# Kernel optimization log

Hardware: AMD Instinct MI355X
Metric: run time of the kernel (lower is better)

The kernel has to match this reference:

```python
import jax, jax.numpy as jnp
import numpy as np

CHANNELS_CHOICE = np.array([8, 16, 24, 32, 40, 48, 56, 64])
MAX_C = 64
B, H, W_SP = 128, 32, 32
N_EDGES = 6
# edge list per intermediate node: (edge_weight_index, source_node_index)
EDGES = [[(0, 0)], [(1, 0), (2, 1)], [(3, 0), (4, 1), (5, 2)]]


def setup_inputs() -> dict:
    key = jax.random.key(0)
    k1, k2, k3, k4 = jax.random.split(key, 4)
    inputs = jax.random.normal(k1, (B, MAX_C, H, W_SP), dtype=jnp.float32)
    alphas1 = jax.random.uniform(k2, (8,), dtype=jnp.float32)  # input-width arch weights
    alphas2 = jax.random.uniform(k3, (8,), dtype=jnp.float32)  # output-width arch weights
    # shared master 3x3 conv weight per edge (OIHW)
    W = jax.random.normal(k4, (N_EDGES, MAX_C, MAX_C, 3, 3), dtype=jnp.float32) * 0.05
    return {"inputs": inputs, "alphas1": alphas1, "alphas2": alphas2, "W": W}


def _channel_scale(alphas1, alphas2, dtype):
    # mask[c, i] = 1 if channel c is inside width choice CHANNELS_CHOICE[i]
    mask = (jnp.arange(MAX_C)[:, None] < jnp.asarray(CHANNELS_CHOICE)[None, :]).astype(dtype)  # [64, 8]
    a_in = mask @ alphas1   # [64] cumulative input-channel weight
    a_out = mask @ alphas2  # [64] cumulative output-channel weight
    return a_out[:, None] * a_in[None, :]  # [64, 64]


def _edge(x, w, scale):
    # weighted-combi of all (c1, c2) channel-sliced sub-convs == one conv with scaled weight
    w_eff = w * scale[:, :, None, None]
    return jax.lax.conv_general_dilated(
        jax.nn.relu(x), w_eff, window_strides=(1, 1), padding="SAME",
        dimension_numbers=("NCHW", "OIHW", "NCHW"))


def reference(inputs, alphas1, alphas2, W):
    scale = _channel_scale(alphas1, alphas2, inputs.dtype)
    nodes = [inputs]
    for node_edges in EDGES:
        feat = 0.0
        for l, src in node_edges:
            feat = feat + _edge(nodes[src], W[l], scale)
        nodes.append(feat)
    return nodes[-1]
```

## Files before the change

kernel.cpp:

```cpp
#include <hip/hip_runtime.h>
#include <hip/hip_bf16.h>


typedef __bf16 bf16x8 __attribute__((ext_vector_type(8)));
typedef float floatx4 __attribute__((ext_vector_type(4)));
typedef unsigned int uint32;

#define PADW 34
#define PIMG (PADW * PADW)
#define ROWB (PADW * 64 * 2)
#define A_LDS (18 * ROWB)
#define A_CHUNKS (A_LDS / 16)
#define A_TAIL (A_CHUNKS - 9 * 512)
#define TAPB (64 * 64 * 2)
#define B_LDS (9 * TAPB)
#define SMEM_BYTES (A_LDS + B_LDS)

__device__ __forceinline__ void gld16(const char* g, char* l) {
    __builtin_amdgcn_global_load_lds(
        (const __attribute__((address_space(1))) uint32*)g,
        (__attribute__((address_space(3))) uint32*)l, 16, 0, 0);
}

__global__ __launch_bounds__(256) void pre_kernel(
    const float* __restrict__ in, const float* __restrict__ a1,
    const float* __restrict__ a2, const float* __restrict__ W,
    __hip_bfloat16* __restrict__ wt, __hip_bfloat16* __restrict__ r0,
    __hip_bfloat16* __restrict__ r1, __hip_bfloat16* __restrict__ r2) {
    __shared__ float tile[32][65];
    int blk = blockIdx.x;
    int tid = threadIdx.x;

    if (blk < 864) {
        int idx = blk * 256 + tid;
        int i = idx & 63;
        int o = (idx >> 6) & 63;
        int rest = idx >> 12;
        int t = rest % 9;
        int l = rest / 9;
        int ji = i >> 3, jo = o >> 3;
        float ain = 0.f, aout = 0.f;
#pragma unroll
        for (int j = 0; j < 8; ++j) {
            ain  += (j >= ji) ? a1[j] : 0.f;
            aout += (j >= jo) ? a2[j] : 0.f;
        }
        float v = W[(size_t)((l * 64 + o) * 64 + i) * 9 + t] * ain * aout;
        int os = ((o & 3) << 4) + (o >> 2);
        size_t e = (size_t)(l * 9 + t) * 4096 + os * 64 +
                   ((((i >> 3) ^ (os & 7)) << 3) + (i & 7));
        wt[e] = __float2bfloat16(v);
    } else if (blk < 992) {
        int b = blk - 864;
        __hip_bfloat16* bufs[3] = {r0, r1, r2};
#pragma unroll
        for (int f = 0; f < 3; ++f) {
            uint32* buf = (uint32*)(bufs[f] + (size_t)b * PIMG * 64);
            for (int idx = tid; idx < 132 * 32; idx += 256) {
                int slot = idx >> 5, u = idx & 31;
                int yy, xx;
                if (slot < 34)      { yy = 0;  xx = slot; }
                else if (slot < 68) { yy = 33; xx = slot - 34; }
                else { int s2 = slot - 68; yy = 1 + (s2 >> 1); xx = (s2 & 1) * 33; }
                buf[(size_t)(yy * PADW + xx) * 32 + u] = 0u;
            }
        }
    } else {
        int rb = blk - 992;
        int b = rb >> 5, y = rb & 31;
        int x = tid & 31, c0 = tid >> 5;
        const float* ip = in + ((size_t)b * 64 * 32 + y) * 32 + x;
#pragma unroll
        for (int cc = 0; cc < 8; ++cc) {
            int c = cc * 8 + c0;
            tile[x][c] = fmaxf(ip[(size_t)c * 1024], 0.f);
        }
        __syncthreads();
        int j = tid & 7, xq = tid >> 3;
        int p = (b * PADW + y + 1) * PADW + 1 + xq;
        alignas(16) __hip_bfloat16 hv[8];
#pragma unroll
        for (int k = 0; k < 8; ++k)
            hv[k] = __float2bfloat16(tile[xq][j * 8 + k]);
        *(uint4*)((char*)r0 + (size_t)p * 128 + ((j ^ (p & 7)) << 4)) =
            *(const uint4*)hv;
    }
}

template <int NSRC, bool FINAL>
__global__ __launch_bounds__(512, 1) void conv_stage(
    const __hip_bfloat16* __restrict__ s0,
    const __hip_bfloat16* __restrict__ s1,
    const __hip_bfloat16* __restrict__ s2,
    const __hip_bfloat16* __restrict__ wt,
    void* __restrict__ dstv, int l0) {
    extern __shared__ char smem[];
    char* smemB = smem + A_LDS;
    int tid = threadIdx.x;
    int wv = tid >> 6, lane = tid & 63;
    int quad = lane >> 4, l15 = lane & 15;
    int blk = blockIdx.x;
    int b = blk >> 1, y0 = (blk & 1) << 4;

    const char* srcs[3] = {(const char*)s0, (const char*)s1, (const char*)s2};
    const char* gW = (const char*)wt + (size_t)l0 * 9 * (size_t)TAPB;
    const size_t aOff = (size_t)(b * PADW + y0) * PADW * 128;

    auto stage_A = [&](int s) {
        const char* gA = srcs[s] + aOff;
#pragma unroll
        for (int it = 0; it < 10; ++it) {
            int c = it * 512 + tid;
            if (it < 9 || tid < A_TAIL)
                gld16(gA + (size_t)c * 16, smem + (it * 512 + wv * 64) * 16);
        }
    };
    auto stage_B = [&](int s) {
        const char* gB = gW + (size_t)s * 9 * TAPB;
#pragma unroll
        for (int it = 0; it < 9; ++it) {
            int c = it * 512 + tid;
            gld16(gB + (size_t)c * 16, smemB + (it * 512 + wv * 64) * 16);
        }
    };

    auto ldA = [&](int tl, int q, bf16x8 (&dst)[4]) {
        const int ky = tl / 3, kx = tl % 3;
#pragma unroll
        for (int m = 0; m < 4; ++m) {
            int arow = 2 * wv + (m >> 1) + ky;
            int apx  = ((m & 1) << 4) + l15 + kx;
            int R = b * PADW + y0 + arow;
            int slot = ((q << 2) + quad) ^ ((2 * R + apx) & 7);
            dst[m] = *(const bf16x8*)(smem + arow * ROWB + apx * 128 +
                                      slot * 16);
        }
    };
    auto ldB = [&](int tl, int q, bf16x8 (&dst)[4]) {
#pragma unroll
        for (int n = 0; n < 4; ++n) {
            int o = (n << 4) + l15;
            int slot = ((q << 2) + quad) ^ (l15 & 7);
            dst[n] = *(const bf16x8*)(smemB + tl * TAPB + o * 128 +
                                      slot * 16);
        }
    };

    floatx4 acc[4][4];
#pragma unroll
    for (int m = 0; m < 4; ++m)
#pragma unroll
        for (int n = 0; n < 4; ++n) acc[m][n] = (floatx4){0.f, 0.f, 0.f, 0.f};

    stage_A(0);
    stage_B(0);
    __syncthreads();

#pragma unroll 1
    for (int s = 0; s < NSRC; ++s) {
        bf16x8 fA[2][4], fB[2][4];
        ldA(0, 0, fA[0]);
        ldB(0, 0, fB[0]);
#pragma unroll
        for (int st = 0; st < 18; ++st) {
            const int pb = st & 1;
            if (st < 17) {
                const int nt = (st + 1) >> 1, nq = (st + 1) & 1;
                ldA(nt, nq, fA[pb ^ 1]);
                ldB(nt, nq, fB[pb ^ 1]);
            }
            __builtin_amdgcn_s_setprio(1);
#pragma unroll
            for (int m = 0; m < 4; ++m)
#pragma unroll
                for (int n = 0; n < 4; ++n)
                    acc[m][n] = __builtin_amdgcn_mfma_f32_16x16x32_bf16(
                        fA[pb][m], fB[pb][n], acc[m][n], 0, 0, 0);
            __builtin_amdgcn_s_setprio(0);
        }
        if (s + 1 < NSRC) {
            __syncthreads();
            stage_A(s + 1);
            stage_B(s + 1);
            __syncthreads();
        }
    }

    if (FINAL) {
        float* out = (float*)dstv;
#pragma unroll
        for (int m = 0; m < 4; ++m) {
            int row = y0 + 2 * wv + (m >> 1);
#pragma unroll
            for (int n = 0; n < 4; ++n) {
                int o = (l15 << 2) + n;
                *(floatx4*)(out + (((size_t)b * 64 + o) * 32 + row) * 32 +
                            ((m & 1) << 4) + (quad << 2)) = acc[m][n];
            }
        }
    } else {
        __hip_bfloat16* out = (__hip_bfloat16*)dstv;
#pragma unroll
        for (int m = 0; m < 4; ++m) {
            int row = y0 + 2 * wv + (m >> 1);
#pragma unroll
            for (int r = 0; r < 4; ++r) {
                int x = ((m & 1) << 4) + (quad << 2) + r;
                int p = (b * PADW + row + 1) * PADW + x + 1;
                alignas(8) __hip_bfloat16 hv[4];
#pragma unroll
                for (int n = 0; n < 4; ++n)
                    hv[n] = __float2bfloat16(fmaxf(acc[m][n][r], 0.f));
                char* d8 = (char*)out + (size_t)p * 128 +
                           ((((l15 >> 1) ^ (p & 7)) << 4) + ((l15 & 1) << 3));
                *(uint2*)d8 = *(const uint2*)hv;
            }
        }
    }
}

extern "C" void kernel_launch(void* const* d_in, const int* in_sizes, int n_in,
                              void* d_out, int out_size, void* d_ws,
                              size_t ws_size, hipStream_t stream) {
    const float* inputs  = (const float*)d_in[0];
    const float* alphas1 = (const float*)d_in[1];
    const float* alphas2 = (const float*)d_in[2];
    const float* W       = (const float*)d_in[3];
    char* ws = (char*)d_ws;

    __hip_bfloat16* wt = (__hip_bfloat16*)(ws);
    __hip_bfloat16* r0 = (__hip_bfloat16*)(ws + ((size_t)1 << 20));
    __hip_bfloat16* r1 = (__hip_bfloat16*)(ws + ((size_t)20 << 20));
    __hip_bfloat16* r2 = (__hip_bfloat16*)(ws + ((size_t)40 << 20));
    float* out = (float*)d_out;

    (void)hipFuncSetAttribute((const void*)conv_stage<1, false>,
                              hipFuncAttributeMaxDynamicSharedMemorySize,
                              SMEM_BYTES);
    (void)hipFuncSetAttribute((const void*)conv_stage<2, false>,
                              hipFuncAttributeMaxDynamicSharedMemorySize,
                              SMEM_BYTES);
    (void)hipFuncSetAttribute((const void*)conv_stage<3, true>,
                              hipFuncAttributeMaxDynamicSharedMemorySize,
                              SMEM_BYTES);

    pre_kernel<<<864 + 128 + 4096, 256, 0, stream>>>(inputs, alphas1, alphas2,
                                                     W, wt, r0, r1, r2);
    conv_stage<1, false><<<256, 512, SMEM_BYTES, stream>>>(r0, r1, r2, wt,
                                                           (void*)r1, 0);
    conv_stage<2, false><<<256, 512, SMEM_BYTES, stream>>>(r0, r1, r2, wt,
                                                           (void*)r2, 1);
    conv_stage<3, true ><<<256, 512, SMEM_BYTES, stream>>>(r0, r1, r2, wt,
                                                           (void*)out, 3);
}
```

Baseline: 148.9 us.

## Fuse input ReLU/bf16 padding conversion into first conv stage

The first conv stage now reads the fp32 input directly, applies ReLU, converts to bf16 in the padded swizzled layout, and writes it to LDS and back to the r0 buffer for later stages. This replaces the 4096 preprocessing blocks in the pre-kernel. It removes a global round trip and part of the pre-kernel work. In exchange, stage 1 staging uses uncoalesced strided fp32 loads instead of async LDS loads.

```diff
diff --git a/kernel.cpp b/kernel.cpp
--- a/kernel.cpp
+++ b/kernel.cpp
@@ -23,11 +23,9 @@
 }
 
 __global__ __launch_bounds__(256) void pre_kernel(
-    const float* __restrict__ in, const float* __restrict__ a1,
-    const float* __restrict__ a2, const float* __restrict__ W,
-    __hip_bfloat16* __restrict__ wt, __hip_bfloat16* __restrict__ r0,
+    const float* __restrict__ a1, const float* __restrict__ a2,
+    const float* __restrict__ W, __hip_bfloat16* __restrict__ wt,
     __hip_bfloat16* __restrict__ r1, __hip_bfloat16* __restrict__ r2) {
-    __shared__ float tile[32][65];
     int blk = blockIdx.x;
     int tid = threadIdx.x;
 
@@ -50,11 +48,11 @@
         size_t e = (size_t)(l * 9 + t) * 4096 + os * 64 +
                    ((((i >> 3) ^ (os & 7)) << 3) + (i & 7));
         wt[e] = __float2bfloat16(v);
-    } else if (blk < 992) {
+    } else {
         int b = blk - 864;
-        __hip_bfloat16* bufs[3] = {r0, r1, r2};
-#pragma unroll
-        for (int f = 0; f < 3; ++f) {
+        __hip_bfloat16* bufs[2] = {r1, r2};
+#pragma unroll
+        for (int f = 0; f < 2; ++f) {
             uint32* buf = (uint32*)(bufs[f] + (size_t)b * PIMG * 64);
             for (int idx = tid; idx < 132 * 32; idx += 256) {
                 int slot = idx >> 5, u = idx & 31;
@@ -65,35 +63,17 @@
                 buf[(size_t)(yy * PADW + xx) * 32 + u] = 0u;
             }
         }
-    } else {
-        int rb = blk - 992;
-        int b = rb >> 5, y = rb & 31;
-        int x = tid & 31, c0 = tid >> 5;
-        const float* ip = in + ((size_t)b * 64 * 32 + y) * 32 + x;
-#pragma unroll
-        for (int cc = 0; cc < 8; ++cc) {
-            int c = cc * 8 + c0;
-            tile[x][c] = fmaxf(ip[(size_t)c * 1024], 0.f);
-        }
-        __syncthreads();
-        int j = tid & 7, xq = tid >> 3;
-        int p = (b * PADW + y + 1) * PADW + 1 + xq;
-        alignas(16) __hip_bfloat16 hv[8];
-#pragma unroll
-        for (int k = 0; k < 8; ++k)
-            hv[k] = __float2bfloat16(tile[xq][j * 8 + k]);
-        *(uint4*)((char*)r0 + (size_t)p * 128 + ((j ^ (p & 7)) << 4)) =
-            *(const uint4*)hv;
     }
 }
 
-template <int NSRC, bool FINAL>
+template <int NSRC, bool FINAL, bool RAW>
 __global__ __launch_bounds__(512, 1) void conv_stage(
     const __hip_bfloat16* __restrict__ s0,
     const __hip_bfloat16* __restrict__ s1,
     const __hip_bfloat16* __restrict__ s2,
     const __hip_bfloat16* __restrict__ wt,
-    void* __restrict__ dstv, int l0) {
+    void* __restrict__ dstv, int l0,
+    const float* __restrict__ rawin, __hip_bfloat16* __restrict__ r0wb) {
     extern __shared__ char smem[];
     char* smemB = smem + A_LDS;
     int tid = threadIdx.x;
@@ -123,6 +103,36 @@
             gld16(gB + (size_t)c * 16, smemB + (it * 512 + wv * 64) * 16);
         }
     };
+    auto stage_raw = [&]() {
+#pragma unroll
+        for (int it = 0; it < 10; ++it) {
+            int c = it * 512 + tid;
+            if (it < 9 || tid < A_TAIL) {
+                int sw = c & 7;
+                int pix = c >> 3;
+                int R = pix / 34, px = pix - R * 34;
+                int P = (b * PADW + y0 + R) * PADW + px;
+                int cb = sw ^ (P & 7);
+                int y = y0 + R - 1, x = px - 1;
+                alignas(16) __hip_bfloat16 hv[8];
+                if ((unsigned)y < 32u && (unsigned)x < 32u) {
+                    const float* ip = rawin +
+                        (((size_t)b * 64 + cb * 8) * 32 + y) * 32 + x;
+#pragma unroll
+                    for (int k = 0; k < 8; ++k)
+                        hv[k] = __float2bfloat16(
+                            fmaxf(ip[(size_t)k * 1024], 0.f));
+                } else {
+#pragma unroll
+                    for (int k = 0; k < 8; ++k)
+                        hv[k] = __float2bfloat16(0.f);
+                }
+                *(uint4*)(smem + (size_t)c * 16) = *(const uint4*)hv;
+                *(uint4*)((char*)r0wb + aOff + (size_t)c * 16) =
+                    *(const uint4*)hv;
+            }
+        }
+    };
 
     auto ldA = [&](int tl, int q, bf16x8 (&dst)[4]) {
         const int ky = tl / 3, kx = tl % 3;
@@ -152,7 +162,7 @@
 #pragma unroll
         for (int n = 0; n < 4; ++n) acc[m][n] = (floatx4){0.f, 0.f, 0.f, 0.f};
 
-    stage_A(0);
+    if constexpr (RAW) stage_raw(); else stage_A(0);
     stage_B(0);
     __syncthreads();
 
@@ -234,22 +244,22 @@
     __hip_bfloat16* r2 = (__hip_bfloat16*)(ws + ((size_t)40 << 20));
     float* out = (float*)d_out;
 
-    (void)hipFuncSetAttribute((const void*)conv_stage<1, false>,
+    (void)hipFuncSetAttribute((const void*)conv_stage<1, false, true>,
                               hipFuncAttributeMaxDynamicSharedMemorySize,
                               SMEM_BYTES);
-    (void)hipFuncSetAttribute((const void*)conv_stage<2, false>,
+    (void)hipFuncSetAttribute((const void*)conv_stage<2, false, false>,
                               hipFuncAttributeMaxDynamicSharedMemorySize,
                               SMEM_BYTES);
-    (void)hipFuncSetAttribute((const void*)conv_stage<3, true>,
+    (void)hipFuncSetAttribute((const void*)conv_stage<3, true, false>,
                               hipFuncAttributeMaxDynamicSharedMemorySize,
                               SMEM_BYTES);
 
-    pre_kernel<<<864 + 128 + 4096, 256, 0, stream>>>(inputs, alphas1, alphas2,
-                                                     W, wt, r0, r1, r2);
-    conv_stage<1, false><<<256, 512, SMEM_BYTES, stream>>>(r0, r1, r2, wt,
-                                                           (void*)r1, 0);
-    conv_stage<2, false><<<256, 512, SMEM_BYTES, stream>>>(r0, r1, r2, wt,
-                                                           (void*)r2, 1);
-    conv_stage<3, true ><<<256, 512, SMEM_BYTES, stream>>>(r0, r1, r2, wt,
-                                                           (void*)out, 3);
-}
+    pre_kernel<<<864 + 128, 256, 0, stream>>>(alphas1, alphas2, W, wt,
+                                              r1, r2);
+    conv_stage<1, false, true><<<256, 512, SMEM_BYTES, stream>>>(
+        r0, r1, r2, wt, (void*)r1, 0, inputs, r0);
+    conv_stage<2, false, false><<<256, 512, SMEM_BYTES, stream>>>(
+        r0, r1, r2, wt, (void*)r2, 1, nullptr, nullptr);
+    conv_stage<3, true, false><<<256, 512, SMEM_BYTES, stream>>>(
+        r0, r1, r2, wt, (void*)out, 3, nullptr, nullptr);
+}
```

New measurement: 161.0 us. 8.1% more time.

## Reorder convs by source node, sharing A tiles across edges with partial-sum buffers

Applied to the files above, without the earlier changes.

Each stage now loads one source node's activation tile once and applies every edge that reads it. A second edge's weights are streamed from global memory in a register-fragment layout (wtR), and its results go into partial-sum buffers (p2, p3) that later stages read back. This cuts redundant reloads of each source tile into LDS and the intra-kernel restaging syncs. In exchange there is extra global traffic for the bf16 partial sums, a second weight layout, and higher register pressure from two accumulator sets. Storing partials in bf16 also adds rounding error.

```diff
diff --git a/kernel.cpp b/kernel.cpp
--- a/kernel.cpp
+++ b/kernel.cpp
@@ -5,6 +5,7 @@
 typedef __bf16 bf16x8 __attribute__((ext_vector_type(8)));
 typedef float floatx4 __attribute__((ext_vector_type(4)));
 typedef unsigned int uint32;
+typedef uint32 u32x4 __attribute__((ext_vector_type(4)));
 
 #define PADW 34
 #define PIMG (PADW * PADW)
@@ -25,8 +26,9 @@
 __global__ __launch_bounds__(256) void pre_kernel(
     const float* __restrict__ in, const float* __restrict__ a1,
     const float* __restrict__ a2, const float* __restrict__ W,
-    __hip_bfloat16* __restrict__ wt, __hip_bfloat16* __restrict__ r0,
-    __hip_bfloat16* __restrict__ r1, __hip_bfloat16* __restrict__ r2) {
+    __hip_bfloat16* __restrict__ wt, __hip_bfloat16* __restrict__ wtR,
+    __hip_bfloat16* __restrict__ r0, __hip_bfloat16* __restrict__ r1,
+    __hip_bfloat16* __restrict__ r2) {
     __shared__ float tile[32][65];
     int blk = blockIdx.x;
     int tid = threadIdx.x;
@@ -49,7 +51,14 @@
         int os = ((o & 3) << 4) + (o >> 2);
         size_t e = (size_t)(l * 9 + t) * 4096 + os * 64 +
                    ((((i >> 3) ^ (os & 7)) << 3) + (i & 7));
-        wt[e] = __float2bfloat16(v);
+        __hip_bfloat16 bv = __float2bfloat16(v);
+        wt[e] = bv;
+        int n  = os >> 4, c15 = os & 15;
+        int q  = i >> 5, quad = (i >> 3) & 3, ee = i & 7;
+        int ln = (quad << 4) + c15;
+        size_t e2 = (size_t)(l * 9 + t) * 4096 + (((q << 2) + n) << 9) +
+                    (ln << 3) + ee;
+        wtR[e2] = bv;
     } else if (blk < 992) {
         int b = blk - 864;
         __hip_bfloat16* bufs[3] = {r0, r1, r2};
@@ -87,13 +96,18 @@
     }
 }
 
-template <int NSRC, bool FINAL>
-__global__ __launch_bounds__(512, 1) void conv_stage(
-    const __hip_bfloat16* __restrict__ s0,
-    const __hip_bfloat16* __restrict__ s1,
-    const __hip_bfloat16* __restrict__ s2,
+#define ZERO4(A_)                                                        \
+    _Pragma("unroll") for (int m_ = 0; m_ < 4; ++m_)                     \
+    _Pragma("unroll") for (int n_ = 0; n_ < 4; ++n_)                     \
+        A_[m_][n_] = (floatx4){0.f, 0.f, 0.f, 0.f};
+
+template <int MODE>
+__global__ __launch_bounds__(512, 1) void conv_k(
+    const __hip_bfloat16* __restrict__ Asrc,
     const __hip_bfloat16* __restrict__ wt,
-    void* __restrict__ dstv, int l0) {
+    const __hip_bfloat16* __restrict__ wtR,
+    __hip_bfloat16* __restrict__ nodeOut, float* __restrict__ finalOut,
+    __hip_bfloat16* __restrict__ p2, __hip_bfloat16* __restrict__ p3) {
     extern __shared__ char smem[];
     char* smemB = smem + A_LDS;
     int tid = threadIdx.x;
@@ -101,13 +115,11 @@
     int quad = lane >> 4, l15 = lane & 15;
     int blk = blockIdx.x;
     int b = blk >> 1, y0 = (blk & 1) << 4;
-
-    const char* srcs[3] = {(const char*)s0, (const char*)s1, (const char*)s2};
-    const char* gW = (const char*)wt + (size_t)l0 * 9 * (size_t)TAPB;
     const size_t aOff = (size_t)(b * PADW + y0) * PADW * 128;
-
-    auto stage_A = [&](int s) {
-        const char* gA = srcs[s] + aOff;
+    const size_t pbase = ((size_t)blk * 512 + tid) << 7;
+
+    auto stage_A = [&]() {
+        const char* gA = (const char*)Asrc + aOff;
 #pragma unroll
         for (int it = 0; it < 10; ++it) {
             int c = it * 512 + tid;
@@ -115,15 +127,14 @@
                 gld16(gA + (size_t)c * 16, smem + (it * 512 + wv * 64) * 16);
         }
     };
-    auto stage_B = [&](int s) {
-        const char* gB = gW + (size_t)s * 9 * TAPB;
+    auto stage_B = [&](int l) {
+        const char* gB = (const char*)wt + (size_t)l * 9 * TAPB;
 #pragma unroll
         for (int it = 0; it < 9; ++it) {
             int c = it * 512 + tid;
             gld16(gB + (size_t)c * 16, smemB + (it * 512 + wv * 64) * 16);
         }
     };
-
     auto ldA = [&](int tl, int q, bf16x8 (&dst)[4]) {
         const int ky = tl / 3, kx = tl % 3;
 #pragma unroll
@@ -145,19 +156,83 @@
                                       slot * 16);
         }
     };
-
-    floatx4 acc[4][4];
-#pragma unroll
-    for (int m = 0; m < 4; ++m)
-#pragma unroll
-        for (int n = 0; n < 4; ++n) acc[m][n] = (floatx4){0.f, 0.f, 0.f, 0.f};
-
-    stage_A(0);
-    stage_B(0);
-    __syncthreads();
-
-#pragma unroll 1
-    for (int s = 0; s < NSRC; ++s) {
+    auto init_p = [&](floatx4 (&acc)[4][4], const __hip_bfloat16* p) {
+#pragma unroll
+        for (int c = 0; c < 8; ++c) {
+            alignas(16) __hip_bfloat16 hv[8];
+            *(uint4*)hv = *(const uint4*)((const char*)p + pbase + c * 16);
+#pragma unroll
+            for (int k = 0; k < 8; ++k) {
+                int j = c * 8 + k;
+                acc[j >> 4][(j >> 2) & 3][j & 3] = __bfloat162float(hv[k]);
+            }
+        }
+    };
+    auto epi_p = [&](floatx4 (&acc)[4][4], __hip_bfloat16* p) {
+#pragma unroll
+        for (int c = 0; c < 8; ++c) {
+            alignas(16) __hip_bfloat16 hv[8];
+#pragma unroll
+            for (int k = 0; k < 8; ++k) {
+                int j = c * 8 + k;
+                hv[k] = __float2bfloat16(acc[j >> 4][(j >> 2) & 3][j & 3]);
+            }
+            *(uint4*)((char*)p + pbase + c * 16) = *(const uint4*)hv;
+        }
+    };
+    auto epi_node = [&](floatx4 (&acc)[4][4], __hip_bfloat16* dst) {
+#pragma unroll
+        for (int m = 0; m < 4; ++m) {
+            int row = y0 + 2 * wv + (m >> 1);
+#pragma unroll
+            for (int r = 0; r < 4; ++r) {
+                int x = ((m & 1) << 4) + (quad << 2) + r;
+                int p = (b * PADW + row + 1) * PADW + x + 1;
+                alignas(8) __hip_bfloat16 hv[4];
+#pragma unroll
+                for (int n = 0; n < 4; ++n)
+                    hv[n] = __float2bfloat16(fmaxf(acc[m][n][r], 0.f));
+                char* d8 = (char*)dst + (size_t)p * 128 +
+                           ((((l15 >> 1) ^ (p & 7)) << 4) + ((l15 & 1) << 3));
+                *(uint2*)d8 = *(const uint2*)hv;
+            }
+        }
+    };
+    auto paired_pass = [&](int lR, floatx4 (&accL)[4][4],
+                           floatx4 (&accR)[4][4]) {
+        const char* gR = (const char*)wtR + (size_t)lR * 9 * TAPB;
+#pragma unroll
+        for (int t = 0; t < 9; ++t) {
+            u32x4 Bb[8];
+#pragma unroll
+            for (int f = 0; f < 8; ++f)
+                Bb[f] = *(const __attribute__((address_space(1))) u32x4*)
+                    (gR + (size_t)t * TAPB + (f << 10) + (lane << 4));
+#pragma unroll
+            for (int q = 0; q < 2; ++q) {
+                bf16x8 Af[4], Bf[4];
+                ldA(t, q, Af);
+                ldB(t, q, Bf);
+                __builtin_amdgcn_s_setprio(1);
+#pragma unroll
+                for (int m = 0; m < 4; ++m)
+#pragma unroll
+                    for (int n = 0; n < 4; ++n)
+                        accL[m][n] = __builtin_amdgcn_mfma_f32_16x16x32_bf16(
+                            Af[m], Bf[n], accL[m][n], 0, 0, 0);
+#pragma unroll
+                for (int n = 0; n < 4; ++n) {
+                    bf16x8 Br = __builtin_bit_cast(bf16x8, Bb[(q << 2) + n]);
+#pragma unroll
+                    for (int m = 0; m < 4; ++m)
+                        accR[m][n] = __builtin_amdgcn_mfma_f32_16x16x32_bf16(
+                            Af[m], Br, accR[m][n], 0, 0, 0);
+                }
+                __builtin_amdgcn_s_setprio(0);
+            }
+        }
+    };
+    auto single_pass = [&](floatx4 (&acc)[4][4]) {
         bf16x8 fA[2][4], fB[2][4];
         ldA(0, 0, fA[0]);
         ldB(0, 0, fB[0]);
@@ -178,42 +253,50 @@
                         fA[pb][m], fB[pb][n], acc[m][n], 0, 0, 0);
             __builtin_amdgcn_s_setprio(0);
         }
-        if (s + 1 < NSRC) {
-            __syncthreads();
-            stage_A(s + 1);
-            stage_B(s + 1);
-            __syncthreads();
-        }
-    }
-
-    if (FINAL) {
-        float* out = (float*)dstv;
+    };
+
+    if constexpr (MODE == 1) {
+        stage_A();
+        stage_B(0);
+        floatx4 aT[4][4], aX[4][4];
+        ZERO4(aT); ZERO4(aX);
+        __syncthreads();
+        paired_pass(1, aT, aX);
+        epi_node(aT, nodeOut);
+        epi_p(aX, p2);
+        __syncthreads();
+        stage_B(3);
+        __syncthreads();
+        floatx4 aY[4][4];
+        ZERO4(aY);
+        single_pass(aY);
+        epi_p(aY, p3);
+    } else if constexpr (MODE == 2) {
+        stage_A();
+        stage_B(2);
+        floatx4 aX[4][4], aY[4][4];
+        init_p(aX, p2);
+        init_p(aY, p3);
+        __syncthreads();
+        paired_pass(4, aX, aY);
+        epi_node(aX, nodeOut);
+        epi_p(aY, p3);
+    } else {
+        stage_A();
+        stage_B(5);
+        floatx4 aY[4][4];
+        init_p(aY, p3);
+        __syncthreads();
+        single_pass(aY);
 #pragma unroll
         for (int m = 0; m < 4; ++m) {
             int row = y0 + 2 * wv + (m >> 1);
 #pragma unroll
             for (int n = 0; n < 4; ++n) {
                 int o = (l15 << 2) + n;
-                *(floatx4*)(out + (((size_t)b * 64 + o) * 32 + row) * 32 +
-                            ((m & 1) << 4) + (quad << 2)) = acc[m][n];
-            }
-        }
-    } else {
-        __hip_bfloat16* out = (__hip_bfloat16*)dstv;
-#pragma unroll
-        for (int m = 0; m < 4; ++m) {
-            int row = y0 + 2 * wv + (m >> 1);
-#pragma unroll
-            for (int r = 0; r < 4; ++r) {
-                int x = ((m & 1) << 4) + (quad << 2) + r;
-                int p = (b * PADW + row + 1) * PADW + x + 1;
-                alignas(8) __hip_bfloat16 hv[4];
-#pragma unroll
-                for (int n = 0; n < 4; ++n)
-                    hv[n] = __float2bfloat16(fmaxf(acc[m][n][r], 0.f));
-                char* d8 = (char*)out + (size_t)p * 128 +
-                           ((((l15 >> 1) ^ (p & 7)) << 4) + ((l15 & 1) << 3));
-                *(uint2*)d8 = *(const uint2*)hv;
+                *(floatx4*)(finalOut +
+                            (((size_t)b * 64 + o) * 32 + row) * 32 +
+                            ((m & 1) << 4) + (quad << 2)) = aY[m][n];
             }
         }
     }
@@ -228,28 +311,31 @@
     const float* W       = (const float*)d_in[3];
     char* ws = (char*)d_ws;
 
-    __hip_bfloat16* wt = (__hip_bfloat16*)(ws);
+    __hip_bfloat16* wt  = (__hip_bfloat16*)(ws);
+    __hip_bfloat16* wtR = (__hip_bfloat16*)(ws + ((size_t)1 << 19));
     __hip_bfloat16* r0 = (__hip_bfloat16*)(ws + ((size_t)1 << 20));
     __hip_bfloat16* r1 = (__hip_bfloat16*)(ws + ((size_t)20 << 20));
     __hip_bfloat16* r2 = (__hip_bfloat16*)(ws + ((size_t)40 << 20));
+    __hip_bfloat16* p2 = (__hip_bfloat16*)(ws + ((size_t)60 << 20));
+    __hip_bfloat16* p3 = (__hip_bfloat16*)(ws + ((size_t)80 << 20));
     float* out = (float*)d_out;
 
-    (void)hipFuncSetAttribute((const void*)conv_stage<1, false>,
+    (void)hipFuncSetAttribute((const void*)conv_k<1>,
                               hipFuncAttributeMaxDynamicSharedMemorySize,
                               SMEM_BYTES);
-    (void)hipFuncSetAttribute((const void*)conv_stage<2, false>,
+    (void)hipFuncSetAttribute((const void*)conv_k<2>,
                               hipFuncAttributeMaxDynamicSharedMemorySize,
                               SMEM_BYTES);
-    (void)hipFuncSetAttribute((const void*)conv_stage<3, true>,
+    (void)hipFuncSetAttribute((const void*)conv_k<3>,
                               hipFuncAttributeMaxDynamicSharedMemorySize,
                               SMEM_BYTES);
 
-    pre_kernel<<<864 + 128 + 4096, 256, 0, stream>>>(inputs, alphas1, alphas2,
-                                                     W, wt, r0, r1, r2);
-    conv_stage<1, false><<<256, 512, SMEM_BYTES, stream>>>(r0, r1, r2, wt,
-                                                           (void*)r1, 0);
-    conv_stage<2, false><<<256, 512, SMEM_BYTES, stream>>>(r0, r1, r2, wt,
-                                                           (void*)r2, 1);
-    conv_stage<3, true ><<<256, 512, SMEM_BYTES, stream>>>(r0, r1, r2, wt,
-                                                           (void*)out, 3);
+    pre_kernel<<<864 + 128 + 4096, 256, 0, stream>>>(
+        inputs, alphas1, alphas2, W, wt, wtR, r0, r1, r2);
+    conv_k<1><<<256, 512, SMEM_BYTES, stream>>>(r0, wt, wtR, r1, nullptr,
+                                                p2, p3);
+    conv_k<2><<<256, 512, SMEM_BYTES, stream>>>(r1, wt, wtR, r2, nullptr,
+                                                p2, p3);
+    conv_k<3><<<256, 512, SMEM_BYTES, stream>>>(r2, wt, wtR, nullptr, out,
+                                                p2, p3);
 }
```

After: 176.6 us. +18.6%, slower.
